# Kernel optimization log

Measured on AMD Instinct MI355X. Metric: run time of the kernel, lower is better.

Reference implementation:

```python
import jax, jax.numpy as jnp
import numpy as np

N, T, D_ENC, D_DEC, U = 32, 2048, 1024, 1024, 1024


def setup_inputs() -> dict:
    key = jax.random.key(0)
    k1, k2, k3, k4, k5, k6 = jax.random.split(key, 6)
    queries = jax.random.normal(k1, (N, 1, D_DEC), dtype=jnp.float32)
    encoder_output = jax.random.normal(k2, (N, T, D_ENC), dtype=jnp.float32)
    # lengths in [1, T] so every row has at least one valid position
    lengths = jax.random.randint(k3, (N,), 1, T + 1, dtype=jnp.int32)
    v = jax.random.normal(k4, (U,), dtype=jnp.float32)
    # torch Linear weights are [out, in]; y = x @ W.T
    Wq = jax.random.normal(k5, (U, D_DEC), dtype=jnp.float32) * (1.0 / np.sqrt(D_DEC))
    Wk = jax.random.normal(k6, (U, D_ENC), dtype=jnp.float32) * (1.0 / np.sqrt(D_ENC))
    return {"queries": queries, "encoder_output": encoder_output,
            "lengths": lengths, "v": v, "Wq": Wq, "Wk": Wk}


def reference(queries, encoder_output, lengths, v, Wq, Wk):
    # set_memory: project keys, build padding mask
    proj_key = jnp.einsum('nte,ue->ntu', encoder_output, Wk)      # [N,T,U]
    mask = jnp.arange(T)[None, :] >= lengths[:, None]             # [N,T] True = masked

    # forward (normalize=False path)
    proj_query = jnp.einsum('nqd,ud->nqu', queries, Wq)           # [N,1,U]
    weights = jnp.tanh(proj_query + proj_key) @ v                 # [N,T]
    weights = jnp.where(mask, -jnp.inf, weights)
    alignments = jax.nn.softmax(weights, axis=-1)                 # [N,T]
    contexts = jnp.einsum('nt,nte->ne', alignments, encoder_output)  # [N,D_enc]
    return contexts, alignments
```

## Files before the change

kernel.cpp:

```cpp
#include <hip/hip_runtime.h>
#include <hip/hip_bf16.h>

#define NB 32
#define TD 2048
#define DIM 1024

typedef _Float16 v8h __attribute__((ext_vector_type(8)));
typedef _Float16 v4h __attribute__((ext_vector_type(4)));
typedef float    v4f __attribute__((ext_vector_type(4)));

__device__ __forceinline__ float ftanh(float x) {
    x = fminf(15.f, fmaxf(-15.f, x));
    float e = __expf(2.f * x);
    return (e - 1.f) / (e + 1.f);
}

__device__ __forceinline__ void gld_lds16(const void* g, void* l) {
    __builtin_amdgcn_global_load_lds(
        (const __attribute__((address_space(1))) unsigned int*)g,
        (__attribute__((address_space(3))) unsigned int*)l, 16, 0, 0);
}

__global__ __launch_bounds__(256) void prep_kernel(
        const float* __restrict__ enc, const float* __restrict__ Wk,
        const float* __restrict__ queries, const float* __restrict__ Wq,
        const int* __restrict__ lengths,
        _Float16* __restrict__ ench, _Float16* __restrict__ wkh,
        float* __restrict__ pq) {
    int bid = blockIdx.x;
    if (bid < 128) {
        int lane = threadIdx.x & 63;
        int wv   = threadIdx.x >> 6;
        int u    = bid * 8 + wv * 2;
        const float* w0 = Wq + (size_t)u * DIM;
        const float* w1 = w0 + DIM;
        float4 wq0[4], wq1[4];
#pragma unroll
        for (int j = 0; j < 4; ++j) {
            wq0[j] = *(const float4*)(w0 + j * 256 + lane * 4);
            wq1[j] = *(const float4*)(w1 + j * 256 + lane * 4);
        }
        for (int n = 0; n < NB; ++n) {
            const float* qn = queries + (size_t)n * DIM;
            float s0 = 0.f, s1 = 0.f;
#pragma unroll
            for (int j = 0; j < 4; ++j) {
                float4 qv = *(const float4*)(qn + j * 256 + lane * 4);
                s0 += qv.x * wq0[j].x + qv.y * wq0[j].y + qv.z * wq0[j].z + qv.w * wq0[j].w;
                s1 += qv.x * wq1[j].x + qv.y * wq1[j].y + qv.z * wq1[j].z + qv.w * wq1[j].w;
            }
#pragma unroll
            for (int off = 32; off >= 1; off >>= 1) {
                s0 += __shfl_xor(s0, off);
                s1 += __shfl_xor(s1, off);
            }
            if (lane == 0) {
                pq[(size_t)n * DIM + u]     = s0;
                pq[(size_t)n * DIM + u + 1] = s1;
            }
        }
        return;
    }
    int cb = bid - 128;
    int local = threadIdx.x * 8;
    int rsub  = local >> 10;
    int col   = local & 1023;
    const float* src;
    _Float16* dst;
    size_t row;
    if (cb < 32768) {
        row = (size_t)cb * 2 + rsub;
        int n = (int)(row >> 11), t = (int)(row & 2047);
        if (t >= lengths[n]) return;
        src = enc; dst = ench;
    } else {
        row = (size_t)(cb - 32768) * 2 + rsub;
        src = Wk; dst = wkh;
    }
    const float4* s = (const float4*)(src + row * DIM + col);
    float4 a = s[0], b = s[1];
    v8h h;
    h[0] = (_Float16)a.x; h[1] = (_Float16)a.y; h[2] = (_Float16)a.z; h[3] = (_Float16)a.w;
    h[4] = (_Float16)b.x; h[5] = (_Float16)b.y; h[6] = (_Float16)b.z; h[7] = (_Float16)b.w;
    *(v8h*)(dst + row * DIM + col) = h;
}

__global__ __launch_bounds__(256) void pq_kernel(const float* __restrict__ q,
                                                 const float* __restrict__ Wq,
                                                 float* __restrict__ pq) {
    int wid  = blockIdx.x * 4 + (threadIdx.x >> 6);
    int lane = threadIdx.x & 63;
    int n = wid >> 10;
    int u = wid & 1023;
    const float4* qr = (const float4*)(q  + (size_t)n * DIM);
    const float4* wr = (const float4*)(Wq + (size_t)u * DIM);
    float s = 0.f;
#pragma unroll
    for (int j = 0; j < 4; ++j) {
        int i = lane + 64 * j;
        float4 a = qr[i], b = wr[i];
        s += a.x * b.x + a.y * b.y + a.z * b.z + a.w * b.w;
    }
#pragma unroll
    for (int off = 32; off >= 1; off >>= 1) s += __shfl_xor(s, off);
    if (lane == 0) pq[(size_t)n * DIM + u] = s;
}

__global__ __launch_bounds__(256) void gemm_tanh_h3(
        const _Float16* __restrict__ ench, const _Float16* __restrict__ wkh,
        const float* __restrict__ pq, const float* __restrict__ v,
        const int* __restrict__ lengths, float* __restrict__ weights) {
    const int bid = blockIdx.x;
    const int xcd = bid & 7;
    const int j   = bid >> 3;
    const int g   = j >> 3;
    const int bm  = (g << 3) | ((xcd ^ g) & 7);
    const int bn  = j & 7;
    const int rowBase = bm * 128;
    const int n = rowBase >> 11;
    const int tstart = rowBase & 2047;
    if (lengths[n] <= tstart) return;

    __shared__ _Float16 As[128 * 64];
    __shared__ _Float16 Bs[128 * 64];

    const int tid  = threadIdx.x;
    const int lane = tid & 63;
    const int wv   = tid >> 6;
    const int wm   = wv >> 1, wn = wv & 1;
    const int q4   = lane >> 4;
    const int l16  = lane & 15;

    float pqv[4], vv[4];
#pragma unroll
    for (int nt = 0; nt < 4; ++nt) {
        int ug = bn * 128 + wn * 64 + nt * 16 + l16;
        pqv[nt] = pq[(size_t)n * DIM + ug];
        vv[nt]  = v[ug];
    }

    const int sr  = lane >> 3;
    const int scs = (lane & 7) ^ sr;

    const _Float16* Ag = ench + (size_t)(rowBase + wv * 32 + sr) * DIM + scs * 8;
    const _Float16* Bg = wkh + (size_t)(bn * 128 + wv * 32 + sr) * DIM + scs * 8;
    _Float16* Al = &As[(wv * 32) * 64];
    _Float16* Bl = &Bs[(wv * 32) * 64];

    v4f acc[4][4];
    const v4f vz = {0.f, 0.f, 0.f, 0.f};
#pragma unroll
    for (int i = 0; i < 4; ++i)
#pragma unroll
        for (int j2 = 0; j2 < 4; ++j2) acc[i][j2] = vz;

    for (int k0 = 0; k0 < DIM; k0 += 64) {
        __syncthreads();
#pragma unroll
        for (int jj = 0; jj < 4; ++jj) {
            gld_lds16(Ag + k0 + jj * 8 * DIM, Al + jj * 8 * 64);
            gld_lds16(Bg + k0 + jj * 8 * DIM, Bl + jj * 8 * 64);
        }
        __syncthreads();

#pragma unroll
        for (int kk = 0; kk < 2; ++kk) {
            v8h a[4], b[4];
#pragma unroll
            for (int mt = 0; mt < 4; ++mt) {
                int r = wm * 64 + mt * 16 + l16;
                a[mt] = *(const v8h*)(&As[r * 64 + (((kk * 4 + q4) ^ (r & 7)) * 8)]);
            }
#pragma unroll
            for (int nt = 0; nt < 4; ++nt) {
                int r = wn * 64 + nt * 16 + l16;
                b[nt] = *(const v8h*)(&Bs[r * 64 + (((kk * 4 + q4) ^ (r & 7)) * 8)]);
            }
#pragma unroll
            for (int mt = 0; mt < 4; ++mt)
#pragma unroll
                for (int nt = 0; nt < 4; ++nt)
                    acc[mt][nt] = __builtin_amdgcn_mfma_f32_16x16x32_f16(
                        a[mt], b[nt], acc[mt][nt], 0, 0, 0);
        }
    }

#pragma unroll
    for (int mt = 0; mt < 4; ++mt) {
#pragma unroll
        for (int r = 0; r < 4; ++r) {
            float s = 0.f;
#pragma unroll
            for (int nt = 0; nt < 4; ++nt)
                s += ftanh(acc[mt][nt][r] + pqv[nt]) * vv[nt];
            s += __shfl_xor(s, 1);
            s += __shfl_xor(s, 2);
            s += __shfl_xor(s, 4);
            s += __shfl_xor(s, 8);
            if (l16 == 0) {
                int R = rowBase + wm * 64 + mt * 16 + q4 * 4 + r;
                atomicAdd(&weights[R], s);
            }
        }
    }
}

__global__ __launch_bounds__(256) void gemm_tanh_kernel(
        const float* __restrict__ enc, const float* __restrict__ Wk,
        const float* __restrict__ pq,  const float* __restrict__ v,
        const int* __restrict__ lengths, float* __restrict__ weights) {
    const int bm = blockIdx.x;
    const int bn = blockIdx.y;
    const int rowBase = bm * 128;
    const int n = rowBase >> 11;
    const int tstart = rowBase & 2047;
    if (lengths[n] <= tstart) return;

    __shared__ _Float16 As[128 * 40];
    __shared__ _Float16 Bs[128 * 40];

    const int tid  = threadIdx.x;
    const int lane = tid & 63;
    const int wv   = tid >> 6;
    const int wm   = wv >> 1, wn = wv & 1;
    const int q4   = lane >> 4;
    const int l16  = lane & 15;

    v4f acc[4][4];
    const v4f vz = {0.f, 0.f, 0.f, 0.f};
#pragma unroll
    for (int i = 0; i < 4; ++i)
#pragma unroll
        for (int j = 0; j < 4; ++j) acc[i][j] = vz;

    const int srow = tid >> 3;
    const int skc  = (tid & 7) * 4;

    for (int k0 = 0; k0 < DIM; k0 += 32) {
        __syncthreads();
#pragma unroll
        for (int j = 0; j < 4; ++j) {
            int row = j * 32 + srow;
            float4 av = *(const float4*)(enc + (size_t)(rowBase + row) * DIM + k0 + skc);
            v4h ah;
            ah.x = (_Float16)av.x; ah.y = (_Float16)av.y;
            ah.z = (_Float16)av.z; ah.w = (_Float16)av.w;
            *(v4h*)(&As[row * 40 + skc]) = ah;
            float4 bv = *(const float4*)(Wk + (size_t)(bn * 128 + row) * DIM + k0 + skc);
            v4h bh;
            bh.x = (_Float16)bv.x; bh.y = (_Float16)bv.y;
            bh.z = (_Float16)bv.z; bh.w = (_Float16)bv.w;
            *(v4h*)(&Bs[row * 40 + skc]) = bh;
        }
        __syncthreads();

        v8h afr[4], bfr[4];
#pragma unroll
        for (int mt = 0; mt < 4; ++mt)
            afr[mt] = *(const v8h*)(&As[(wm * 64 + mt * 16 + l16) * 40 + q4 * 8]);
#pragma unroll
        for (int nt = 0; nt < 4; ++nt)
            bfr[nt] = *(const v8h*)(&Bs[(wn * 64 + nt * 16 + l16) * 40 + q4 * 8]);
#pragma unroll
        for (int mt = 0; mt < 4; ++mt)
#pragma unroll
            for (int nt = 0; nt < 4; ++nt)
                acc[mt][nt] = __builtin_amdgcn_mfma_f32_16x16x32_f16(
                    afr[mt], bfr[nt], acc[mt][nt], 0, 0, 0);
    }

    float pqv[4], vv[4];
#pragma unroll
    for (int nt = 0; nt < 4; ++nt) {
        int ug = bn * 128 + wn * 64 + nt * 16 + l16;
        pqv[nt] = pq[(size_t)n * DIM + ug];
        vv[nt]  = v[ug];
    }
#pragma unroll
    for (int mt = 0; mt < 4; ++mt) {
#pragma unroll
        for (int r = 0; r < 4; ++r) {
            float s = 0.f;
#pragma unroll
            for (int nt = 0; nt < 4; ++nt)
                s += ftanh(acc[mt][nt][r] + pqv[nt]) * vv[nt];
            s += __shfl_xor(s, 1);
            s += __shfl_xor(s, 2);
            s += __shfl_xor(s, 4);
            s += __shfl_xor(s, 8);
            if (l16 == 0) {
                int R = rowBase + wm * 64 + mt * 16 + q4 * 4 + r;
                atomicAdd(&weights[R], s);
            }
        }
    }
}

__global__ __launch_bounds__(256) void softmax_kernel(float* __restrict__ w,
                                                      const int* __restrict__ lengths) {
    int n = blockIdx.x;
    int len = lengths[n];
    float* row = w + (size_t)n * TD;
    int tid = threadIdx.x;
    float wv[8], ev[8];
    float mx = -INFINITY;
#pragma unroll
    for (int i = 0; i < 8; ++i) {
        int t = tid + i * 256;
        float x = row[t];
        x = (t < len) ? x : -INFINITY;
        wv[i] = x;
        mx = fmaxf(mx, x);
    }
#pragma unroll
    for (int off = 32; off >= 1; off >>= 1) mx = fmaxf(mx, __shfl_xor(mx, off));
    __shared__ float redm[4], reds[4];
    int lane = tid & 63, wvid = tid >> 6;
    if (lane == 0) redm[wvid] = mx;
    __syncthreads();
    mx = fmaxf(fmaxf(redm[0], redm[1]), fmaxf(redm[2], redm[3]));
    float sm = 0.f;
#pragma unroll
    for (int i = 0; i < 8; ++i) { ev[i] = __expf(wv[i] - mx); sm += ev[i]; }
#pragma unroll
    for (int off = 32; off >= 1; off >>= 1) sm += __shfl_xor(sm, off);
    if (lane == 0) reds[wvid] = sm;
    __syncthreads();
    sm = reds[0] + reds[1] + reds[2] + reds[3];
    float inv = 1.f / sm;
#pragma unroll
    for (int i = 0; i < 8; ++i) row[tid + i * 256] = ev[i] * inv;
}

__global__ __launch_bounds__(256) void ctx_kernel_h4(const float* __restrict__ align,
                                                     const _Float16* __restrict__ ench,
                                                     const int* __restrict__ lengths,
                                                     float* __restrict__ ctx) {
    int n  = blockIdx.y;
    int t0 = blockIdx.x * 64;
    int len = lengths[n];
    if (len <= t0) return;
    int half = threadIdx.x >> 7;
    int col  = (threadIdx.x & 127) * 8;
    float acc[8];
#pragma unroll
    for (int i = 0; i < 8; ++i) acc[i] = 0.f;
    int tend = min(t0 + 64, len);
    const float* arow = align + (size_t)n * TD;
    const _Float16* ebase = ench + (size_t)n * TD * DIM + col;
#pragma unroll 2
    for (int t = t0 + half; t < tend; t += 2) {
        float a = arow[t];
        v8h e = *(const v8h*)(ebase + (size_t)t * DIM);
#pragma unroll
        for (int i = 0; i < 8; ++i) acc[i] += a * (float)e[i];
    }
    __shared__ float cred[DIM];
    if (half == 1) {
#pragma unroll
        for (int i = 0; i < 8; ++i) cred[col + i] = acc[i];
    }
    __syncthreads();
    if (half == 0) {
        float* c = ctx + (size_t)n * DIM + col;
#pragma unroll
        for (int i = 0; i < 8; ++i) atomicAdd(c + i, acc[i] + cred[col + i]);
    }
}

__global__ __launch_bounds__(256) void ctx_kernel(const float* __restrict__ align,
                                                  const float* __restrict__ enc,
                                                  const int* __restrict__ lengths,
                                                  float* __restrict__ ctx) {
    int n  = blockIdx.y;
    int t0 = blockIdx.x * 128;
    if (lengths[n] <= t0) return;
    int e = threadIdx.x * 4;
    float4 acc = make_float4(0.f, 0.f, 0.f, 0.f);
    const float* arow = align + (size_t)n * TD;
    const float* erow = enc + (size_t)n * TD * DIM;
    for (int tt = 0; tt < 128; ++tt) {
        int t = t0 + tt;
        float a = arow[t];
        if (a != 0.f) {
            float4 evv = *(const float4*)(erow + (size_t)t * DIM + e);
            acc.x += a * evv.x; acc.y += a * evv.y;
            acc.z += a * evv.z; acc.w += a * evv.w;
        }
    }
    float* c = ctx + (size_t)n * DIM + e;
    atomicAdd(c + 0, acc.x);
    atomicAdd(c + 1, acc.y);
    atomicAdd(c + 2, acc.z);
    atomicAdd(c + 3, acc.w);
}

extern "C" void kernel_launch(void* const* d_in, const int* in_sizes, int n_in,
                              void* d_out, int out_size, void* d_ws, size_t ws_size,
                              hipStream_t stream) {
    const float* queries = (const float*)d_in[0];
    const float* enc     = (const float*)d_in[1];
    const int*   lengths = (const int*)d_in[2];
    const float* v       = (const float*)d_in[3];
    const float* Wq      = (const float*)d_in[4];
    const float* Wk      = (const float*)d_in[5];

    float* out = (float*)d_out;
    float* ctx = out;
    float* alg = out + NB * DIM;
    float* pq  = ctx;
    (void)in_sizes; (void)n_in; (void)out_size;

    const size_t ench_elems = (size_t)NB * TD * DIM;
    const size_t need = (ench_elems + (size_t)DIM * DIM) * sizeof(_Float16);

    hipMemsetAsync(alg, 0, (size_t)NB * TD * sizeof(float), stream);

    if (ws_size >= need) {
        _Float16* ench = (_Float16*)d_ws;
        _Float16* wkh  = ench + ench_elems;
        prep_kernel<<<128 + 32768 + 512, 256, 0, stream>>>(
            enc, Wk, queries, Wq, lengths, ench, wkh, pq);
        gemm_tanh_h3<<<4096, 256, 0, stream>>>(ench, wkh, pq, v, lengths, alg);
        softmax_kernel<<<NB, 256, 0, stream>>>(alg, lengths);
        hipMemsetAsync(ctx, 0, (size_t)NB * DIM * sizeof(float), stream);
        ctx_kernel_h4<<<dim3(32, NB), 256, 0, stream>>>(alg, ench, lengths, ctx);
    } else {
        pq_kernel<<<NB * DIM / 4, 256, 0, stream>>>(queries, Wq, pq);
        dim3 g2(512, 8);
        gemm_tanh_kernel<<<g2, 256, 0, stream>>>(enc, Wk, pq, v, lengths, alg);
        softmax_kernel<<<NB, 256, 0, stream>>>(alg, lengths);
        hipMemsetAsync(ctx, 0, (size_t)NB * DIM * sizeof(float), stream);
        ctx_kernel<<<dim3(16, NB), 256, 0, stream>>>(alg, enc, lengths, ctx);
    }
}
```

Baseline: 501.5 us.

## Rewrite tanh-GEMM as 256x256 tile, 8-wave kernel with multi-buffered LDS pipeline

Replaces the 128x128 tile, 4-wave GEMM with a 256x256 tile, 512-thread kernel. The new kernel uses a 4-slot LDS ring, prefetches the next K tiles with async global-to-LDS loads interleaved among MFMA phases, and uses partial vmcnt waits, sched barriers and setprio around the MFMA blocks. The aim is to overlap global loads with compute and to raise data reuse per block, cutting both the sync stalls and the global traffic of the old two-barrier-per-K-step loop. The cost is higher register and LDS use per block, which lowers occupancy, and coarser length-based skipping because tiles now span 256 rows.

```diff
diff --git a/kernel.cpp b/kernel.cpp
--- a/kernel.cpp
+++ b/kernel.cpp
@@ -4,6 +4,7 @@
 #define NB 32
 #define TD 2048
 #define DIM 1024
+#define NT 16
 
 typedef _Float16 v8h __attribute__((ext_vector_type(8)));
 typedef _Float16 v4h __attribute__((ext_vector_type(4)));
@@ -20,6 +21,10 @@
         (const __attribute__((address_space(1))) unsigned int*)g,
         (__attribute__((address_space(3))) unsigned int*)l, 16, 0, 0);
 }
+
+#define SBAR() do { __builtin_amdgcn_sched_barrier(0); \
+                    __builtin_amdgcn_s_barrier(); \
+                    __builtin_amdgcn_sched_barrier(0); } while (0)
 
 __global__ __launch_bounds__(256) void prep_kernel(
         const float* __restrict__ enc, const float* __restrict__ Wk,
@@ -106,87 +111,121 @@
     if (lane == 0) pq[(size_t)n * DIM + u] = s;
 }
 
-__global__ __launch_bounds__(256) void gemm_tanh_h3(
+__global__ __launch_bounds__(512, 2) void gemm_tanh_8p(
         const _Float16* __restrict__ ench, const _Float16* __restrict__ wkh,
         const float* __restrict__ pq, const float* __restrict__ v,
         const int* __restrict__ lengths, float* __restrict__ weights) {
     const int bid = blockIdx.x;
     const int xcd = bid & 7;
     const int j   = bid >> 3;
-    const int g   = j >> 3;
+    const int g   = j >> 2;
     const int bm  = (g << 3) | ((xcd ^ g) & 7);
-    const int bn  = j & 7;
-    const int rowBase = bm * 128;
+    const int bn  = j & 3;
+    const int rowBase = bm * 256;
     const int n = rowBase >> 11;
     const int tstart = rowBase & 2047;
     if (lengths[n] <= tstart) return;
-
-    __shared__ _Float16 As[128 * 64];
-    __shared__ _Float16 Bs[128 * 64];
+    const int bnBase = bn * 256;
+
+    __shared__ _Float16 Asl[4 * 128 * 64];
+    __shared__ _Float16 Bsl[4 * 128 * 64];
 
     const int tid  = threadIdx.x;
     const int lane = tid & 63;
     const int wv   = tid >> 6;
-    const int wm   = wv >> 1, wn = wv & 1;
+    const int wm   = wv >> 2;
+    const int wn   = wv & 3;
     const int q4   = lane >> 4;
     const int l16  = lane & 15;
+    const int sr   = lane >> 3;
+    const int scs  = (lane & 7) ^ sr;
+
+    auto STAGE_A = [&](int tile, int h) {
+        const _Float16* src = ench + (size_t)(rowBase + h * 128 + wv * 16 + sr) * DIM
+                              + tile * 64 + scs * 8;
+        _Float16* dst = Asl + ((2 * tile + h) & 3) * (128 * 64) + (wv * 16) * 64;
+        gld_lds16(src, dst);
+        gld_lds16(src + (size_t)8 * DIM, dst + 8 * 64);
+    };
+    auto STAGE_B = [&](int tile, int h) {
+        const _Float16* src = wkh + (size_t)(bnBase + h * 128 + wv * 16 + sr) * DIM
+                              + tile * 64 + scs * 8;
+        _Float16* dst = Bsl + ((2 * tile + h) & 3) * (128 * 64) + (wv * 16) * 64;
+        gld_lds16(src, dst);
+        gld_lds16(src + (size_t)8 * DIM, dst + 8 * 64);
+    };
+
+    v4f acc[8][4];
+    const v4f vz = {0.f, 0.f, 0.f, 0.f};
+#pragma unroll
+    for (int i = 0; i < 8; ++i)
+#pragma unroll
+        for (int k = 0; k < 4; ++k) acc[i][k] = vz;
+
+    STAGE_A(0, 0); STAGE_A(0, 1); STAGE_B(0, 0); STAGE_B(0, 1); STAGE_B(1, 0);
+    asm volatile("s_waitcnt vmcnt(2)" ::: "memory");
+    SBAR();
+
+    for (int t = 0; t < NT; ++t) {
+        v8h breg[2][4];
+#pragma unroll
+        for (int p = 0; p < 4; ++p) {
+            v8h a[2][2];
+            {
+                const _Float16* Ab = Asl + ((2 * t + wm) & 3) * (128 * 64);
+#pragma unroll
+                for (int ml = 0; ml < 2; ++ml) {
+                    int rl = p * 32 + ml * 16 + l16;
+                    int sw = rl & 7;
+                    a[0][ml] = *(const v8h*)(Ab + rl * 64 + ((q4 ^ sw) * 8));
+                    a[1][ml] = *(const v8h*)(Ab + rl * 64 + (((4 + q4) ^ sw) * 8));
+                }
+            }
+            if (p == 0) {
+                const _Float16* Bb = Bsl + ((2 * t + (wn >> 1)) & 3) * (128 * 64);
+#pragma unroll
+                for (int nt = 0; nt < 4; ++nt) {
+                    int rl = (wn & 1) * 64 + nt * 16 + l16;
+                    int sw = rl & 7;
+                    breg[0][nt] = *(const v8h*)(Bb + rl * 64 + ((q4 ^ sw) * 8));
+                    breg[1][nt] = *(const v8h*)(Bb + rl * 64 + (((4 + q4) ^ sw) * 8));
+                }
+            }
+            if (p == 0)      { if (t + 1 < NT) STAGE_A(t + 1, 0); }
+            else if (p == 1) { if (t + 1 < NT) STAGE_A(t + 1, 1); }
+            else if (p == 2) { if (t + 1 < NT) STAGE_B(t + 1, 1); }
+            else             { if (t + 2 < NT) STAGE_B(t + 2, 0); }
+
+            SBAR();
+            __builtin_amdgcn_s_setprio(1);
+#pragma unroll
+            for (int ml = 0; ml < 2; ++ml)
+#pragma unroll
+                for (int nt = 0; nt < 4; ++nt) {
+                    acc[p * 2 + ml][nt] = __builtin_amdgcn_mfma_f32_16x16x32_f16(
+                        a[0][ml], breg[0][nt], acc[p * 2 + ml][nt], 0, 0, 0);
+                    acc[p * 2 + ml][nt] = __builtin_amdgcn_mfma_f32_16x16x32_f16(
+                        a[1][ml], breg[1][nt], acc[p * 2 + ml][nt], 0, 0, 0);
+                }
+            __builtin_amdgcn_s_setprio(0);
+            if (p < 3) SBAR();
+        }
+        if (t < NT - 1) {
+            if (t + 2 < NT) { asm volatile("s_waitcnt vmcnt(2)" ::: "memory"); }
+            else            { asm volatile("s_waitcnt vmcnt(0)" ::: "memory"); }
+            SBAR();
+        }
+    }
 
     float pqv[4], vv[4];
 #pragma unroll
     for (int nt = 0; nt < 4; ++nt) {
-        int ug = bn * 128 + wn * 64 + nt * 16 + l16;
+        int ug = bnBase + wn * 64 + nt * 16 + l16;
         pqv[nt] = pq[(size_t)n * DIM + ug];
         vv[nt]  = v[ug];
     }
-
-    const int sr  = lane >> 3;
-    const int scs = (lane & 7) ^ sr;
-
-    const _Float16* Ag = ench + (size_t)(rowBase + wv * 32 + sr) * DIM + scs * 8;
-    const _Float16* Bg = wkh + (size_t)(bn * 128 + wv * 32 + sr) * DIM + scs * 8;
-    _Float16* Al = &As[(wv * 32) * 64];
-    _Float16* Bl = &Bs[(wv * 32) * 64];
-
-    v4f acc[4][4];
-    const v4f vz = {0.f, 0.f, 0.f, 0.f};
-#pragma unroll
-    for (int i = 0; i < 4; ++i)
-#pragma unroll
-        for (int j2 = 0; j2 < 4; ++j2) acc[i][j2] = vz;
-
-    for (int k0 = 0; k0 < DIM; k0 += 64) {
-        __syncthreads();
-#pragma unroll
-        for (int jj = 0; jj < 4; ++jj) {
-            gld_lds16(Ag + k0 + jj * 8 * DIM, Al + jj * 8 * 64);
-            gld_lds16(Bg + k0 + jj * 8 * DIM, Bl + jj * 8 * 64);
-        }
-        __syncthreads();
-
-#pragma unroll
-        for (int kk = 0; kk < 2; ++kk) {
-            v8h a[4], b[4];
-#pragma unroll
-            for (int mt = 0; mt < 4; ++mt) {
-                int r = wm * 64 + mt * 16 + l16;
-                a[mt] = *(const v8h*)(&As[r * 64 + (((kk * 4 + q4) ^ (r & 7)) * 8)]);
-            }
-#pragma unroll
-            for (int nt = 0; nt < 4; ++nt) {
-                int r = wn * 64 + nt * 16 + l16;
-                b[nt] = *(const v8h*)(&Bs[r * 64 + (((kk * 4 + q4) ^ (r & 7)) * 8)]);
-            }
-#pragma unroll
-            for (int mt = 0; mt < 4; ++mt)
-#pragma unroll
-                for (int nt = 0; nt < 4; ++nt)
-                    acc[mt][nt] = __builtin_amdgcn_mfma_f32_16x16x32_f16(
-                        a[mt], b[nt], acc[mt][nt], 0, 0, 0);
-        }
-    }
-
-#pragma unroll
-    for (int mt = 0; mt < 4; ++mt) {
+#pragma unroll
+    for (int mt = 0; mt < 8; ++mt) {
 #pragma unroll
         for (int r = 0; r < 4; ++r) {
             float s = 0.f;
@@ -198,7 +237,7 @@
             s += __shfl_xor(s, 4);
             s += __shfl_xor(s, 8);
             if (l16 == 0) {
-                int R = rowBase + wm * 64 + mt * 16 + q4 * 4 + r;
+                int R = rowBase + wm * 128 + mt * 16 + q4 * 4 + r;
                 atomicAdd(&weights[R], s);
             }
         }
@@ -421,7 +460,7 @@
         _Float16* wkh  = ench + ench_elems;
         prep_kernel<<<128 + 32768 + 512, 256, 0, stream>>>(
             enc, Wk, queries, Wq, lengths, ench, wkh, pq);
-        gemm_tanh_h3<<<4096, 256, 0, stream>>>(ench, wkh, pq, v, lengths, alg);
+        gemm_tanh_8p<<<1024, 512, 0, stream>>>(ench, wkh, pq, v, lengths, alg);
         softmax_kernel<<<NB, 256, 0, stream>>>(alg, lengths);
         hipMemsetAsync(ctx, 0, (size_t)NB * DIM * sizeof(float), stream);
         ctx_kernel_h4<<<dim3(32, NB), 256, 0, stream>>>(alg, ench, lengths, ctx);
```

New measurement: 513.4 us. +2.4%, slower.
